# Performance work log

Measured on AMD Instinct MI355X. Metric: run time of the kernel, lower is better.

The kernel has to match this reference:

```python
import jax, jax.numpy as jnp
import numpy as np

# snntorch Leaky defaults / CFG constants
BETA = 0.9      # CFG.lif_beta
IAPP = 0.0      # CFG.Iapp
THR = 1.0       # snn.Leaky default threshold
SLOPE = 25.0    # surrogate.fast_sigmoid default slope


@jax.custom_vjp
def spike(x):
    # Heaviside spike with fast-sigmoid surrogate gradient
    return (x > 0).astype(x.dtype)

def _spike_fwd(x):
    return spike(x), x

def _spike_bwd(x, g):
    return (g / (SLOPE * jnp.abs(x) + 1.0) ** 2,)

spike.defvjp(_spike_fwd, _spike_bwd)


def setup_inputs() -> dict:
    key = jax.random.key(0)
    z = jax.random.normal(key, (32, 1024, 512), dtype=jnp.float32)
    return {"z": z}


def reference(z):
    # z: [B, T, H]; sequential LIF over time axis.
    # snntorch Leaky (reset='subtract'):
    #   reset = detach(V_prev > thr)
    #   V_k   = beta * V_prev + input_k - reset * thr
    #   spk_k = heaviside(V_k - thr)
    # Original loop: input at step k is z[:, k-1] + Iapp (noise std = 0.0).
    B, T, H = z.shape
    zt = jnp.transpose(z[:, :-1, :], (1, 0, 2))  # [T-1, B, H]
    V0 = jnp.zeros((B, H), dtype=z.dtype)

    def step(V, zin):
        reset = jax.lax.stop_gradient((V > THR).astype(V.dtype))
        Vn = BETA * V + (zin + IAPP) - reset * THR
        spk = spike(Vn - THR)
        return Vn, spk

    _, spks = jax.lax.scan(step, V0, zt)  # spks: [T-1, B, H]
    # T[:, 0, :] stays zero (loop starts at k=1)
    Tout = jnp.concatenate(
        [jnp.zeros((B, 1, H), dtype=z.dtype), jnp.transpose(spks, (1, 0, 2))],
        axis=1,
    )
    return Tout
```

## Files before the change

### kernel.cpp

```cpp
#include <hip/hip_runtime.h>


#define LIF_B 32
#define LIF_T 1024
#define LIF_H 512
#define LIF_S 1023
#define LIF_P 31

__global__ __launch_bounds__(64) void lif_kernel(const float* __restrict__ z,
                                                 float* __restrict__ out) {
    const int n = blockIdx.x * blockDim.x + threadIdx.x;
    const int b = n >> 9;
    const int h = n & (LIF_H - 1);
    const int base = b * (LIF_T * LIF_H) + h;

    out[base] = 0.0f;

    float buf[LIF_P];
#pragma unroll
    for (int i = 0; i < LIF_P; ++i)
        buf[i] = z[base + i * LIF_H];

    float V = 0.0f;
    int t = 0;
    for (int blk = 0; blk < 32; ++blk) {
#pragma unroll
        for (int i = 0; i < LIF_P; ++i) {
            const float zv = buf[i];
            buf[i] = z[base + (t + LIF_P) * LIF_H];
            const float v0 = __fadd_rn(__fmul_rn(0.9f, V), zv);
            const float Vn = (V > 1.0f) ? __fsub_rn(v0, 1.0f) : v0;
            out[base + (t + 1) * LIF_H] = (Vn > 1.0f) ? 1.0f : 0.0f;
            V = Vn;
            ++t;
        }
    }
#pragma unroll
    for (int i = 0; i < LIF_P; ++i) {
        const float zv = buf[i];
        const float v0 = __fadd_rn(__fmul_rn(0.9f, V), zv);
        const float Vn = (V > 1.0f) ? __fsub_rn(v0, 1.0f) : v0;
        out[base + (t + 1) * LIF_H] = (Vn > 1.0f) ? 1.0f : 0.0f;
        V = Vn;
        ++t;
    }
}

extern "C" void kernel_launch(void* const* d_in, const int* in_sizes, int n_in,
                              void* d_out, int out_size, void* d_ws, size_t ws_size,
                              hipStream_t stream) {
    const float* z = (const float*)d_in[0];
    float* out = (float*)d_out;
    const int total = LIF_B * LIF_H;
    dim3 block(64);
    dim3 grid(total / 64);
    hipLaunchKernelGGL(lif_kernel, grid, block, 0, stream, z, out);
}
```

Measured before the change: 135.4 us.

## Stream z through double-buffered LDS via async global_load_lds DMA

Replaces the per-thread 31-deep register prefetch ring with a block-level double buffer in shared memory. Asynchronous global_load_lds copies each 64-timestep by 64-neuron tile while the previous tile is consumed, with hand-coded waitcnt values to synchronise. This aims to hide global load latency behind the serial recurrence with larger, more coalesced transfers. The hard-coded waitcnt encodings and the missing barriers between waves are fragile, and launch bounds limit the kernel to one block per CU setting.

Measured after the change: 139.1 us. 2.7% more time.

```diff
diff --git a/kernel.cpp b/kernel.cpp
--- a/kernel.cpp
+++ b/kernel.cpp
@@ -1,48 +1,76 @@
 #include <hip/hip_runtime.h>
 
 
-#define LIF_B 32
-#define LIF_T 1024
 #define LIF_H 512
-#define LIF_S 1023
-#define LIF_P 31
 
-__global__ __launch_bounds__(64) void lif_kernel(const float* __restrict__ z,
-                                                 float* __restrict__ out) {
-    const int n = blockIdx.x * blockDim.x + threadIdx.x;
-    const int b = n >> 9;
-    const int h = n & (LIF_H - 1);
-    const int base = b * (LIF_T * LIF_H) + h;
+typedef __attribute__((address_space(3))) void lds_void_t;
+typedef const __attribute__((address_space(1))) void gbl_void_t;
+#define DMA16(gp, lp) \
+    __builtin_amdgcn_global_load_lds((gbl_void_t*)(gp), (lds_void_t*)(lp), 16, 0, 0)
 
-    out[base] = 0.0f;
+#define WAIT_VM16() __builtin_amdgcn_s_waitcnt(0x4F70)
+#define WAIT_VM0()  __builtin_amdgcn_s_waitcnt(0x0F70)
 
-    float buf[LIF_P];
+__global__ __launch_bounds__(64, 1) void lif_kernel(const float* __restrict__ z,
+                                                    float* __restrict__ out) {
+    __shared__ float bufA[64 * 64];
+    __shared__ float bufB[64 * 64];
+
+    const int tid = threadIdx.x;
+    const int blk = blockIdx.x;
+    const int b = blk >> 3;
+    const int h0 = (blk & 7) << 6;
+    const size_t base = (size_t)b * (1024 * LIF_H) + h0;
+
+    const float* zb = z + base;
+    float* op = out + base + tid;
+
+    op[0] = 0.0f;
+
+    const float* gsrc = zb + (tid >> 4) * LIF_H + (tid & 15) * 4;
+
 #pragma unroll
-    for (int i = 0; i < LIF_P; ++i)
-        buf[i] = z[base + i * LIF_H];
+    for (int j = 0; j < 16; ++j)
+        DMA16(gsrc + j * (4 * LIF_H), bufA + j * 256);
 
     float V = 0.0f;
-    int t = 0;
-    for (int blk = 0; blk < 32; ++blk) {
+    for (int p = 0; p < 8; ++p) {
+        const int c0 = 2 * p;
+
 #pragma unroll
-        for (int i = 0; i < LIF_P; ++i) {
-            const float zv = buf[i];
-            buf[i] = z[base + (t + LIF_P) * LIF_H];
+        for (int j = 0; j < 16; ++j)
+            DMA16(gsrc + (size_t)(c0 + 1) * (64 * LIF_H) + j * (4 * LIF_H),
+                  bufB + j * 256);
+        WAIT_VM16();
+
+#pragma unroll 4
+        for (int s = 0; s < 64; ++s) {
+            const float zv = bufA[s * 64 + tid];
             const float v0 = __fadd_rn(__fmul_rn(0.9f, V), zv);
             const float Vn = (V > 1.0f) ? __fsub_rn(v0, 1.0f) : v0;
-            out[base + (t + 1) * LIF_H] = (Vn > 1.0f) ? 1.0f : 0.0f;
+            op[(size_t)(c0 * 64 + s + 1) * LIF_H] = (Vn > 1.0f) ? 1.0f : 0.0f;
             V = Vn;
-            ++t;
         }
-    }
+
+        if (p < 7) {
 #pragma unroll
-    for (int i = 0; i < LIF_P; ++i) {
-        const float zv = buf[i];
-        const float v0 = __fadd_rn(__fmul_rn(0.9f, V), zv);
-        const float Vn = (V > 1.0f) ? __fsub_rn(v0, 1.0f) : v0;
-        out[base + (t + 1) * LIF_H] = (Vn > 1.0f) ? 1.0f : 0.0f;
-        V = Vn;
-        ++t;
+            for (int j = 0; j < 16; ++j)
+                DMA16(gsrc + (size_t)(c0 + 2) * (64 * LIF_H) + j * (4 * LIF_H),
+                      bufA + j * 256);
+            WAIT_VM16();
+        } else {
+            WAIT_VM0();
+        }
+
+        const int smax = (p < 7) ? 64 : 63;
+#pragma unroll 4
+        for (int s = 0; s < smax; ++s) {
+            const float zv = bufB[s * 64 + tid];
+            const float v0 = __fadd_rn(__fmul_rn(0.9f, V), zv);
+            const float Vn = (V > 1.0f) ? __fsub_rn(v0, 1.0f) : v0;
+            op[(size_t)((c0 + 1) * 64 + s + 1) * LIF_H] = (Vn > 1.0f) ? 1.0f : 0.0f;
+            V = Vn;
+        }
     }
 }
 
@@ -51,8 +79,7 @@
                               hipStream_t stream) {
     const float* z = (const float*)d_in[0];
     float* out = (float*)d_out;
-    const int total = LIF_B * LIF_H;
     dim3 block(64);
-    dim3 grid(total / 64);
+    dim3 grid(256);
     hipLaunchKernelGGL(lif_kernel, grid, block, 0, stream, z, out);
 }
```

## Split time axis into segments with warmup recomputation for more parallelism

Applied to the files above, without the earlier changes.

Splits the 1023-step recurrence into 8 time segments, one per block group, so eight times as many threads run concurrently. Each segment starts from V=0 and replays up to 512 earlier steps to warm the state, relying on the 0.9 decay to converge V before it emits spikes. This shortens the serial dependency chain per thread and raises occupancy. In exchange it re-reads much of the input several times. Exactness also depends on the warmup converging, because the reset and spike threshold are discontinuous.

New measurement: 176.3 us. 1.3x slower.

```diff
diff --git a/kernel.cpp b/kernel.cpp
--- a/kernel.cpp
+++ b/kernel.cpp
@@ -1,48 +1,45 @@
 #include <hip/hip_runtime.h>
 
 
-#define LIF_B 32
-#define LIF_T 1024
 #define LIF_H 512
-#define LIF_S 1023
-#define LIF_P 31
+#define SEG   128
+#define WARM  512
 
-__global__ __launch_bounds__(64) void lif_kernel(const float* __restrict__ z,
-                                                 float* __restrict__ out) {
-    const int n = blockIdx.x * blockDim.x + threadIdx.x;
-    const int b = n >> 9;
-    const int h = n & (LIF_H - 1);
-    const int base = b * (LIF_T * LIF_H) + h;
+__global__ __launch_bounds__(256, 2) void lif_kernel(const float* __restrict__ z,
+                                                     float* __restrict__ out) {
+    const int beta = blockIdx.x;
+    const int half = beta & 1;
+    const int g    = (beta >> 1) & 7;
+    const int b    = beta >> 4;
+    const int h    = (half << 8) + threadIdx.x;
+    const size_t base = (size_t)b * (1024 * LIF_H) + h;
 
-    out[base] = 0.0f;
+    const float* zp = z + base;
+    float* op = out + base;
 
-    float buf[LIF_P];
-#pragma unroll
-    for (int i = 0; i < LIF_P; ++i)
-        buf[i] = z[base + i * LIF_H];
+    const int s_begin = g * SEG;
+    const int s_end   = (g == 7) ? 1023 : s_begin + SEG;
+    int s0 = s_begin - WARM;
+    if (s0 < 0) s0 = 0;
 
     float V = 0.0f;
-    int t = 0;
-    for (int blk = 0; blk < 32; ++blk) {
-#pragma unroll
-        for (int i = 0; i < LIF_P; ++i) {
-            const float zv = buf[i];
-            buf[i] = z[base + (t + LIF_P) * LIF_H];
-            const float v0 = __fadd_rn(__fmul_rn(0.9f, V), zv);
-            const float Vn = (V > 1.0f) ? __fsub_rn(v0, 1.0f) : v0;
-            out[base + (t + 1) * LIF_H] = (Vn > 1.0f) ? 1.0f : 0.0f;
-            V = Vn;
-            ++t;
-        }
+
+#pragma unroll 8
+    for (int s = s0; s < s_begin; ++s) {
+        const float zv = zp[(size_t)s * LIF_H];
+        const float v0 = __fadd_rn(__fmul_rn(0.9f, V), zv);
+        V = (V > 1.0f) ? __fsub_rn(v0, 1.0f) : v0;
     }
-#pragma unroll
-    for (int i = 0; i < LIF_P; ++i) {
-        const float zv = buf[i];
+
+    if (g == 0) op[0] = 0.0f;
+
+#pragma unroll 4
+    for (int s = s_begin; s < s_end; ++s) {
+        const float zv = zp[(size_t)s * LIF_H];
         const float v0 = __fadd_rn(__fmul_rn(0.9f, V), zv);
         const float Vn = (V > 1.0f) ? __fsub_rn(v0, 1.0f) : v0;
-        out[base + (t + 1) * LIF_H] = (Vn > 1.0f) ? 1.0f : 0.0f;
+        op[(size_t)(s + 1) * LIF_H] = (Vn > 1.0f) ? 1.0f : 0.0f;
         V = Vn;
-        ++t;
     }
 }
 
@@ -51,8 +48,7 @@
                               hipStream_t stream) {
     const float* z = (const float*)d_in[0];
     float* out = (float*)d_out;
-    const int total = LIF_B * LIF_H;
-    dim3 block(64);
-    dim3 grid(total / 64);
+    dim3 block(256);
+    dim3 grid(512);
     hipLaunchKernelGGL(lif_kernel, grid, block, 0, stream, z, out);
 }
```

## Stage time chunks through double-buffered LDS with batched register prefetch

Applied to the files above, without the earlier changes.

Replaces the per-step rolling register prefetch with chunked loads of 32 timesteps into registers, which are then written to alternating shared-memory buffers. The recurrence for the current chunk reads from LDS while the next chunk's global loads are in flight. This aims to batch memory requests and overlap load latency with the sequential scan. It adds LDS writes and reads per element, and the loads are issued in bursts rather than a steady stream.

After: 132.8 us. Within noise of the previous version (-1.9%).

```diff
diff --git a/kernel.cpp b/kernel.cpp
--- a/kernel.cpp
+++ b/kernel.cpp
@@ -1,48 +1,62 @@
 #include <hip/hip_runtime.h>
 
 
-#define LIF_B 32
-#define LIF_T 1024
 #define LIF_H 512
-#define LIF_S 1023
-#define LIF_P 31
+#define TS 32
 
-__global__ __launch_bounds__(64) void lif_kernel(const float* __restrict__ z,
-                                                 float* __restrict__ out) {
-    const int n = blockIdx.x * blockDim.x + threadIdx.x;
-    const int b = n >> 9;
-    const int h = n & (LIF_H - 1);
-    const int base = b * (LIF_T * LIF_H) + h;
+__global__ __launch_bounds__(64, 1) void lif_kernel(const float* __restrict__ z,
+                                                    float* __restrict__ out) {
+    __shared__ float Abuf[TS * 64];
+    __shared__ float Bbuf[TS * 64];
 
-    out[base] = 0.0f;
+    const int t = threadIdx.x;
+    const int blk = blockIdx.x;
+    const int b = blk >> 3;
+    const int h0 = (blk & 7) << 6;
+    const size_t base = (size_t)b * (1024 * LIF_H) + h0 + t;
 
-    float buf[LIF_P];
+    const float* zp = z + base;
+    float* op = out + base;
+
+    op[0] = 0.0f;
+
+    float r[TS];
+
 #pragma unroll
-    for (int i = 0; i < LIF_P; ++i)
-        buf[i] = z[base + i * LIF_H];
+    for (int j = 0; j < TS; ++j) r[j] = zp[(size_t)j * LIF_H];
+#pragma unroll
+    for (int j = 0; j < TS; ++j) Abuf[j * 64 + t] = r[j];
 
     float V = 0.0f;
-    int t = 0;
-    for (int blk = 0; blk < 32; ++blk) {
+
+    for (int k = 0; k < 31; ++k) {
+        const float* cur = (k & 1) ? Bbuf : Abuf;
+        float* nxt = (k & 1) ? Abuf : Bbuf;
+
 #pragma unroll
-        for (int i = 0; i < LIF_P; ++i) {
-            const float zv = buf[i];
-            buf[i] = z[base + (t + LIF_P) * LIF_H];
+        for (int j = 0; j < TS; ++j)
+            r[j] = zp[(size_t)((k + 1) * TS + j) * LIF_H];
+
+#pragma unroll
+        for (int i = 0; i < TS; ++i) {
+            const float zv = cur[i * 64 + t];
             const float v0 = __fadd_rn(__fmul_rn(0.9f, V), zv);
             const float Vn = (V > 1.0f) ? __fsub_rn(v0, 1.0f) : v0;
-            out[base + (t + 1) * LIF_H] = (Vn > 1.0f) ? 1.0f : 0.0f;
+            op[(size_t)(k * TS + i + 1) * LIF_H] = (Vn > 1.0f) ? 1.0f : 0.0f;
             V = Vn;
-            ++t;
         }
+
+#pragma unroll
+        for (int j = 0; j < TS; ++j) nxt[j * 64 + t] = r[j];
     }
+
 #pragma unroll
-    for (int i = 0; i < LIF_P; ++i) {
-        const float zv = buf[i];
+    for (int i = 0; i < TS - 1; ++i) {
+        const float zv = Bbuf[i * 64 + t];
         const float v0 = __fadd_rn(__fmul_rn(0.9f, V), zv);
         const float Vn = (V > 1.0f) ? __fsub_rn(v0, 1.0f) : v0;
-        out[base + (t + 1) * LIF_H] = (Vn > 1.0f) ? 1.0f : 0.0f;
+        op[(size_t)(31 * TS + i + 1) * LIF_H] = (Vn > 1.0f) ? 1.0f : 0.0f;
         V = Vn;
-        ++t;
     }
 }
 
@@ -51,8 +65,7 @@
                               hipStream_t stream) {
     const float* z = (const float*)d_in[0];
     float* out = (float*)d_out;
-    const int total = LIF_B * LIF_H;
     dim3 block(64);
-    dim3 grid(total / 64);
+    dim3 grid(256);
     hipLaunchKernelGGL(lif_kernel, grid, block, 0, stream, z, out);
 }
```
